# Kernel tuning notes

Measured on AMD Instinct MI355X. Metric: run time of the kernel, lower is better.

The kernel has to match this reference:

```python
import jax, jax.numpy as jnp
import numpy as np

B, D, NB, BS = 32, 2048, 16, 512  # batch, dim_input=dim_output, n_blocks, block_size; NB*BS*BS == D*D


def setup_inputs() -> dict:
    key = jax.random.key(0)
    k1, k2, k3, k4, k5 = jax.random.split(key, 5)
    x = jax.random.normal(k1, (B, D), dtype=jnp.float32)
    gate_w = jax.random.normal(k2, (D, NB), dtype=jnp.float32) / np.sqrt(D)
    gate_b = jax.random.normal(k3, (NB,), dtype=jnp.float32) * 0.02
    weight = jax.random.normal(k4, (D, D), dtype=jnp.float32) / np.sqrt(D)  # kaiming-uniform-like scale
    bias = jax.random.normal(k5, (D,), dtype=jnp.float32) * (1.0 / np.sqrt(D))
    return {"x": x, "gate_w": gate_w, "gate_b": gate_b, "weight": weight, "bias": bias}


def reference(x, gate_w, gate_b, weight, bias):
    b = x.shape[0]
    k_drop = NB // 2
    # gate network: Linear -> Sigmoid
    g = jax.nn.sigmoid(x @ gate_w + gate_b)  # (b, NB)
    # zero out the k smallest gates per sample (topk largest=False, scatter 0)
    _, drop_idx = jax.lax.top_k(-g, k_drop)  # indices of smallest gates
    rows = jnp.arange(b)[:, None]
    g = g.at[rows, drop_idx].set(0.0)
    # broadcast gates over block-diagonal chunks of weight
    w0 = weight.reshape(NB, BS, BS)
    gw = (g[:, :, None, None] * w0).reshape(b, D, D)  # (b, dim_output, dim_input)
    # batched matvec + bias
    return jnp.einsum('bij,bj->bi', gw, x) + bias
```

## Files before the change

kernel.cpp:

```cpp
#include <hip/hip_runtime.h>
#include <hip/hip_bf16.h>


#define D_DIM 2048
#define B_DIM 32
#define NB_DIM 16
#define KSPLIT 8
#define KCHUNK (D_DIM / KSPLIT)

typedef __attribute__((ext_vector_type(4))) float f32x4;
typedef __attribute__((ext_vector_type(8))) float f32x8;
typedef __attribute__((ext_vector_type(8))) __bf16 bf16x8;

static __device__ __forceinline__ __bf16 f2bf(float f) {
    unsigned u = __builtin_bit_cast(unsigned, f);
    u += 0x7fffu + ((u >> 16) & 1u);
    unsigned short h = (unsigned short)(u >> 16);
    return __builtin_bit_cast(__bf16, h);
}

static __device__ __forceinline__ bf16x8 load_cvt8(const float* p) {
    const f32x8 v = *(const f32x8*)p;
    bf16x8 r;
#pragma unroll
    for (int i = 0; i < 8; ++i) r[i] = f2bf(v[i]);
    return r;
}

__global__ __launch_bounds__(256) void prep_kernel(
    const float* __restrict__ X,
    const float* __restrict__ GW,
    const float* __restrict__ GB,
    float* __restrict__ gates,
    __bf16* __restrict__ Xbf)
{
    __shared__ float red[NB_DIM][256];
    __shared__ float sg[NB_DIM];
    const int b = blockIdx.x;
    const int t = threadIdx.x;

    {
        const int idx = b * D_DIM + t * 8;
        *(bf16x8*)(Xbf + idx) = load_cvt8(X + idx);
    }

    float acc[NB_DIM];
#pragma unroll
    for (int n = 0; n < NB_DIM; ++n) acc[n] = 0.f;

#pragma unroll
    for (int i = 0; i < D_DIM / 256; ++i) {
        const int c = t + i * 256;
        const float xv = X[b * D_DIM + c];
        const float* gw = GW + c * NB_DIM;
#pragma unroll
        for (int n = 0; n < NB_DIM; ++n) acc[n] += xv * gw[n];
    }
#pragma unroll
    for (int n = 0; n < NB_DIM; ++n) red[n][t] = acc[n];
    __syncthreads();
    for (int s = 128; s > 0; s >>= 1) {
        if (t < s) {
#pragma unroll
            for (int n = 0; n < NB_DIM; ++n) red[n][t] += red[n][t + s];
        }
        __syncthreads();
    }
    if (t < NB_DIM) {
        const float v = red[t][0] + GB[t];
        sg[t] = 1.f / (1.f + __expf(-v));
    }
    __syncthreads();
    if (t < NB_DIM) {
        const float g = sg[t];
        int rank = 0;
#pragma unroll
        for (int m = 0; m < NB_DIM; ++m) {
            const float gm = sg[m];
            if (gm < g || (gm == g && m < t)) rank++;
        }
        gates[b * NB_DIM + t] = (rank >= NB_DIM / 2) ? g : 0.f;
    }
}

__global__ __launch_bounds__(256) void main_gemm(
    const float* __restrict__ W,
    const __bf16* __restrict__ Xbf,
    float* __restrict__ part)
{
    const int bid  = blockIdx.x;
    const int ks   = bid & (KSPLIT - 1);
    const int rg   = bid >> 3;
    const int wave = threadIdx.x >> 6;
    const int lane = threadIdx.x & 63;
    const int l15  = lane & 15;
    const int q    = lane >> 4;

    const int r0 = rg * 64 + wave * 16;
    const int k0 = ks * KCHUNK;

    const float*  arow = W   + (size_t)(r0 + l15) * D_DIM + k0 + q * 8;
    const __bf16* b0p  = Xbf + (size_t)(l15)      * D_DIM + k0 + q * 8;
    const __bf16* b1p  = Xbf + (size_t)(l15 + 16) * D_DIM + k0 + q * 8;

    f32x4 acc0 = {0.f, 0.f, 0.f, 0.f};
    f32x4 acc1 = {0.f, 0.f, 0.f, 0.f};

#pragma unroll
    for (int kk = 0; kk < KCHUNK / 32; ++kk) {
        const bf16x8 av  = load_cvt8(arow + kk * 32);
        const bf16x8 bv0 = *(const bf16x8*)(b0p + kk * 32);
        const bf16x8 bv1 = *(const bf16x8*)(b1p + kk * 32);
        acc0 = __builtin_amdgcn_mfma_f32_16x16x32_bf16(av, bv0, acc0, 0, 0, 0);
        acc1 = __builtin_amdgcn_mfma_f32_16x16x32_bf16(av, bv1, acc1, 0, 0, 0);
    }

    float* p0 = part + (size_t)ks * (B_DIM * D_DIM) + (size_t)l15 * D_DIM        + r0 + q * 4;
    float* p1 = part + (size_t)ks * (B_DIM * D_DIM) + (size_t)(l15 + 16) * D_DIM + r0 + q * 4;
    *(f32x4*)p0 = acc0;
    *(f32x4*)p1 = acc1;
}

__global__ __launch_bounds__(256) void reduce_kernel(
    const float* __restrict__ part,
    const float* __restrict__ gates,
    const float* __restrict__ bias,
    float* __restrict__ out)
{
    const int t   = blockIdx.x * 256 + threadIdx.x;
    const int idx = t * 4;
    const int b   = idx >> 11;
    const int r   = idx & (D_DIM - 1);

    f32x4 s = {0.f, 0.f, 0.f, 0.f};
#pragma unroll
    for (int ks = 0; ks < KSPLIT; ++ks) {
        s += *(const f32x4*)(part + (size_t)ks * (B_DIM * D_DIM) + idx);
    }
    const float g = gates[b * NB_DIM + (r >> 7)];
    const f32x4 bi = *(const f32x4*)(bias + r);

    f32x4 y;
#pragma unroll
    for (int i = 0; i < 4; ++i) y[i] = g * s[i] + bi[i];
    *(f32x4*)(out + idx) = y;
}

extern "C" void kernel_launch(void* const* d_in, const int* in_sizes, int n_in,
                              void* d_out, int out_size, void* d_ws, size_t ws_size,
                              hipStream_t stream) {
    const float* x    = (const float*)d_in[0];
    const float* gw   = (const float*)d_in[1];
    const float* gb   = (const float*)d_in[2];
    const float* w    = (const float*)d_in[3];
    const float* bias = (const float*)d_in[4];
    float* out = (float*)d_out;

    float*  part  = (float*)d_ws;
    float*  gates = (float*)((char*)d_ws + 2097152);
    __bf16* Xbf   = (__bf16*)((char*)d_ws + 2097152 + 4096);

    prep_kernel<<<B_DIM, 256, 0, stream>>>(x, gw, gb, gates, Xbf);
    main_gemm<<<32 * KSPLIT, 256, 0, stream>>>(w, Xbf, part);
    reduce_kernel<<<(B_DIM * D_DIM) / (256 * 4), 256, 0, stream>>>(part, gates, bias, out);
}
```

Measured before the change: 83.07 us.

## Fuse split-K reduction into GEMM via shared-memory wave reduction

Replaces the separate split-K partial-sum buffer and reduce kernel with one fused kernel. Each 512-thread block computes 16 output rows, and its 8 waves split K and reduce their partials through padded LDS before applying gate and bias. This removes one kernel launch and the 2 MB partial write and read through global memory, at the cost of a block-wide sync and a smaller grid of 128 blocks.

After: 83.88 us. Within noise of the previous version (+1.0%).

```diff
diff --git a/kernel.cpp b/kernel.cpp
--- a/kernel.cpp
+++ b/kernel.cpp
@@ -5,8 +5,9 @@
 #define D_DIM 2048
 #define B_DIM 32
 #define NB_DIM 16
-#define KSPLIT 8
-#define KCHUNK (D_DIM / KSPLIT)
+#define NWAVE 8
+#define KCHUNK (D_DIM / NWAVE)
+#define PM_PAD 20
 
 typedef __attribute__((ext_vector_type(4))) float f32x4;
 typedef __attribute__((ext_vector_type(8))) float f32x8;
@@ -83,21 +84,23 @@
     }
 }
 
-__global__ __launch_bounds__(256) void main_gemm(
+__global__ __launch_bounds__(512) void main_fused(
     const float* __restrict__ W,
     const __bf16* __restrict__ Xbf,
-    float* __restrict__ part)
+    const float* __restrict__ gates,
+    const float* __restrict__ bias,
+    float* __restrict__ out)
 {
-    const int bid  = blockIdx.x;
-    const int ks   = bid & (KSPLIT - 1);
-    const int rg   = bid >> 3;
+    __shared__ float pm[NWAVE * B_DIM * PM_PAD];
+
+    const int rt   = blockIdx.x;
     const int wave = threadIdx.x >> 6;
     const int lane = threadIdx.x & 63;
     const int l15  = lane & 15;
     const int q    = lane >> 4;
 
-    const int r0 = rg * 64 + wave * 16;
-    const int k0 = ks * KCHUNK;
+    const int r0 = rt * 16;
+    const int k0 = wave * KCHUNK;
 
     const float*  arow = W   + (size_t)(r0 + l15) * D_DIM + k0 + q * 8;
     const __bf16* b0p  = Xbf + (size_t)(l15)      * D_DIM + k0 + q * 8;
@@ -115,35 +118,22 @@
         acc1 = __builtin_amdgcn_mfma_f32_16x16x32_bf16(av, bv1, acc1, 0, 0, 0);
     }
 
-    float* p0 = part + (size_t)ks * (B_DIM * D_DIM) + (size_t)l15 * D_DIM        + r0 + q * 4;
-    float* p1 = part + (size_t)ks * (B_DIM * D_DIM) + (size_t)(l15 + 16) * D_DIM + r0 + q * 4;
-    *(f32x4*)p0 = acc0;
-    *(f32x4*)p1 = acc1;
-}
+    float* base = pm + wave * (B_DIM * PM_PAD);
+    *(f32x4*)(base + l15 * PM_PAD + q * 4)        = acc0;
+    *(f32x4*)(base + (l15 + 16) * PM_PAD + q * 4) = acc1;
+    __syncthreads();
 
-__global__ __launch_bounds__(256) void reduce_kernel(
-    const float* __restrict__ part,
-    const float* __restrict__ gates,
-    const float* __restrict__ bias,
-    float* __restrict__ out)
-{
-    const int t   = blockIdx.x * 256 + threadIdx.x;
-    const int idx = t * 4;
-    const int b   = idx >> 11;
-    const int r   = idx & (D_DIM - 1);
+    const int t   = threadIdx.x;
+    const int lb  = t >> 4;
+    const int row = t & 15;
+    float s = 0.f;
+#pragma unroll
+    for (int w = 0; w < NWAVE; ++w)
+        s += pm[w * (B_DIM * PM_PAD) + lb * PM_PAD + row];
 
-    f32x4 s = {0.f, 0.f, 0.f, 0.f};
-#pragma unroll
-    for (int ks = 0; ks < KSPLIT; ++ks) {
-        s += *(const f32x4*)(part + (size_t)ks * (B_DIM * D_DIM) + idx);
-    }
-    const float g = gates[b * NB_DIM + (r >> 7)];
-    const f32x4 bi = *(const f32x4*)(bias + r);
-
-    f32x4 y;
-#pragma unroll
-    for (int i = 0; i < 4; ++i) y[i] = g * s[i] + bi[i];
-    *(f32x4*)(out + idx) = y;
+    const float g  = gates[lb * NB_DIM + (r0 >> 7)];
+    const float bi = bias[r0 + row];
+    out[(size_t)lb * D_DIM + r0 + row] = g * s + bi;
 }
 
 extern "C" void kernel_launch(void* const* d_in, const int* in_sizes, int n_in,
@@ -156,11 +146,9 @@
     const float* bias = (const float*)d_in[4];
     float* out = (float*)d_out;
 
-    float*  part  = (float*)d_ws;
-    float*  gates = (float*)((char*)d_ws + 2097152);
-    __bf16* Xbf   = (__bf16*)((char*)d_ws + 2097152 + 4096);
+    float*  gates = (float*)d_ws;
+    __bf16* Xbf   = (__bf16*)((char*)d_ws + 4096);
 
     prep_kernel<<<B_DIM, 256, 0, stream>>>(x, gw, gb, gates, Xbf);
-    main_gemm<<<32 * KSPLIT, 256, 0, stream>>>(w, Xbf, part);
-    reduce_kernel<<<(B_DIM * D_DIM) / (256 * 4), 256, 0, stream>>>(part, gates, bias, out);
+    main_fused<<<D_DIM / 16, 512, 0, stream>>>(w, Xbf, gates, bias, out);
 }
```
